# Optimization experiments

Hardware: AMD Instinct MI355X
Metric: run time of the kernel (lower is better)

Reference implementation:

```python
import jax, jax.numpy as jnp
import numpy as np

SPATIAL = (14, 14)
FEATURE_DIM = 768
N, T, H, D = 16, 8, 12, 64
L = SPATIAL[0] * SPATIAL[1] + 1  # 197 (cls token + 196 patches)
W_SIZE = (2 * SPATIAL[0] - 1) * (2 * SPATIAL[1] - 1)  # 729


def _build_idx():
    # relative-position index map [196, 196], matches the torch double loop
    hs, ws = SPATIAL
    pos = np.arange(hs * ws)
    pi, pj = pos // ws, pos % ws
    i_offs = pi[:, None] - pi[None, :] + hs - 1
    j_offs = pj[:, None] - pj[None, :] + ws - 1
    return jnp.asarray(i_offs * (2 * ws - 1) + j_offs, dtype=jnp.int32)


def setup_inputs() -> dict:
    key = jax.random.key(0)
    kq, kk, kw1, kw2 = jax.random.split(key, 4)
    q = jax.random.normal(kq, (N, T, L, H, D), dtype=jnp.float32)
    k = jax.random.normal(kk, (N, T, L, H, D), dtype=jnp.float32)
    # learned relative-position bias tables (zeros in torch init; use small random for a meaningful baseline)
    w1 = jax.random.normal(kw1, (W_SIZE, FEATURE_DIM), dtype=jnp.float32) * 0.02
    w2 = jax.random.normal(kw2, (W_SIZE, FEATURE_DIM), dtype=jnp.float32) * 0.02
    idx = _build_idx()
    return {"q": q, "k": k, "w1": w1, "w2": w2, "idx": idx}


def _forward_half(q, k, w, idx):
    # q, k: [N, T', L, H, D]; strip cls token -> [N, T', 196, H, D]
    q = q[:, :, 1:]
    k = k[:, :, 1:]
    scale = 1.0 / jnp.sqrt(jnp.asarray(q.shape[-1], q.dtype))
    attn = jnp.einsum('ntqhd,ntkhd->ntqkh', q * scale, k)
    attn = jax.nn.softmax(attn, axis=-2).mean(axis=-1)  # [N, T', 196, 196]
    w_unroll = w[idx]  # gather: [196, 196, C]
    return jnp.einsum('ntqk,qkc->ntqc', attn, w_unroll)


def reference(q, k, w1, w2, idx):
    n, t, l, _, _ = q.shape
    c = w1.shape[-1]
    ret = jnp.zeros((n, t, l, c), dtype=q.dtype)
    ret = ret.at[:, 1:, 1:, :].add(_forward_half(q[:, 1:], k[:, :-1], w1, idx))
    ret = ret.at[:, :-1, 1:, :].add(_forward_half(q[:, :-1], k[:, 1:], w2, idx))
    return ret
```

## Files before the change

### kernel.cpp

```cpp
#include <hip/hip_runtime.h>

#define N_ 16
#define T_ 8
#define L_ 197
#define H_ 12
#define D_ 64
#define Q_ 196
#define C_ 768
#define KP 224
#define ENT 1792
#define ATS 216
#define APLANE 2112

typedef unsigned short ushort_t;
typedef __bf16 bf16x8 __attribute__((ext_vector_type(8)));
typedef float floatx4 __attribute__((ext_vector_type(4)));

#define GLD_LDS16(g, l)                                                    \
  __builtin_amdgcn_global_load_lds(                                        \
      (const __attribute__((address_space(1))) void*)(g),                  \
      (__attribute__((address_space(3))) void*)(l), 16, 0, 0)

static __device__ inline ushort_t f2bf(float x) {
  unsigned int u = __float_as_uint(x);
  u += 0x7fffu + ((u >> 16) & 1u);
  return (ushort_t)(u >> 16);
}
static __device__ inline unsigned int pack2(float a, float b) {
  return (unsigned int)f2bf(a) | ((unsigned int)f2bf(b) << 16);
}

__global__ __launch_bounds__(256, 4) void convert_kernel(
    const float* __restrict__ q, const float* __restrict__ k,
    uint4* __restrict__ qb, uint4* __restrict__ kb) {
  const int nt  = blockIdx.x;
  const int h   = blockIdx.y;
  const int inp = blockIdx.z;
  const int tid = threadIdx.x;

  const float* src = inp ? k : q;
  const float sc = inp ? 1.f : 0.125f;
  uint4* dst = (inp ? kb : qb) + ((size_t)nt * H_ + h) * ENT;

  __shared__ __align__(16) uint4 lds[8 * KP];

  const float* base = src + ((size_t)nt * L_ + 1) * (H_ * D_) + h * D_;

  float4 va[7], vb[7];
  #pragma unroll
  for (int r = 0; r < 7; r++) {
    int e = tid + 256 * r;
    int pos = e >> 3, dc = e & 7;
    if (r < 6 || tid < 32) {
      const float* p = base + (size_t)pos * (H_ * D_) + dc * 8;
      va[r] = *(const float4*)p;
      vb[r] = *(const float4*)(p + 4);
    }
  }
  __builtin_amdgcn_sched_barrier(0);

  #pragma unroll
  for (int r = 0; r < 7; r++) {
    int e = tid + 256 * r;
    int pos = e >> 3, dc = e & 7;
    if (r < 6 || tid < 32) {
      uint4 o;
      o.x = pack2(va[r].x * sc, va[r].y * sc);
      o.y = pack2(va[r].z * sc, va[r].w * sc);
      o.z = pack2(vb[r].x * sc, vb[r].y * sc);
      o.w = pack2(vb[r].z * sc, vb[r].w * sc);
      lds[dc * KP + ((pos & ~7) | ((pos ^ dc) & 7))] = o;
    }
  }
  __syncthreads();

  #pragma unroll
  for (int r = 0; r < 7; r++) {
    int e = tid + 256 * r;
    int dc = e / KP, pos = e - dc * KP;
    uint4 v;
    if (pos < 196) v = lds[dc * KP + ((pos & ~7) | ((pos ^ dc) & 7))];
    else           v = (uint4){0u, 0u, 0u, 0u};
    dst[e] = v;
  }
}

__global__ __launch_bounds__(256, 2) void attn_kernel(
    const uint4* __restrict__ qb, const uint4* __restrict__ kb,
    ushort_t* __restrict__ A1, ushort_t* __restrict__ A2) {
  const int lin  = blockIdx.x;
  const int xcd  = lin & 7;
  const int slot = lin >> 3;
  const int g    = (slot >> 2) * 8 + xcd;
  const int b    = slot & 3;
  const int half = g / 112;
  const int nt   = g - half * 112;
  const int n  = nt / 7, tp = nt % 7;
  const int tq = (half == 0) ? tp + 1 : tp;
  const int tk = (half == 0) ? tp     : tp + 1;
  const int ntq = n * T_ + tq;
  const int ntk = n * T_ + tk;

  const uint4* qpl = qb + (size_t)ntq * H_ * ENT;
  const uint4* kpl = kb + (size_t)ntk * H_ * ENT;
  ushort_t* Ah = (half == 0) ? A1 : A2;

  __shared__ __align__(16) uint4 ks[2][ENT];
  ushort_t* at = (ushort_t*)ks;

  const int tid  = threadIdx.x;
  const int lane = tid & 63;
  const int wv   = tid >> 6;
  const int quad = lane >> 4;
  const int l15  = lane & 15;
  const int qi_b = 64 * b + 16 * wv;

  float accA[13][4];
  #pragma unroll
  for (int t = 0; t < 13; t++)
    #pragma unroll
    for (int r = 0; r < 4; r++) accA[t][r] = 0.f;

  auto stage = [&](int h, uint4* bufp) {
    #pragma unroll
    for (int r = 0; r < 7; r++)
      GLD_LDS16(kpl + (size_t)h * ENT + 256 * r + 64 * wv + lane,
                (char*)bufp + (256 * r + 64 * wv) * 16);
  };
  auto loadq = [&](int h, bf16x8* qf) {
    #pragma unroll
    for (int kk = 0; kk < 2; kk++)
      qf[kk] = *(const bf16x8*)&qpl[(size_t)h * ENT + (quad + 4 * kk) * KP + qi_b + l15];
  };

  auto headbody = [&](int h, uint4* bufp, bf16x8* qf, bool lastwait) {
    if (lastwait) asm volatile("s_waitcnt vmcnt(0)" ::: "memory");
    else          asm volatile("s_waitcnt vmcnt(9)" ::: "memory");
    __builtin_amdgcn_s_barrier();
    asm volatile("" ::: "memory");

    const ushort_t* bu = (const ushort_t*)bufp;
    floatx4 S[13];
    #pragma unroll
    for (int t = 0; t < 13; t++) S[t] = (floatx4){0.f, 0.f, 0.f, 0.f};
    #pragma unroll
    for (int kk = 0; kk < 2; kk++)
      #pragma unroll
      for (int t = 0; t < 13; t++) {
        bf16x8 bbv = *(const bf16x8*)&bu[((quad + 4 * kk) * KP + 16 * t + l15) * 8];
        S[t] = __builtin_amdgcn_mfma_f32_16x16x32_bf16(qf[kk], bbv, S[t], 0, 0, 0);
      }

    asm volatile("" ::: "memory");
    __builtin_amdgcn_s_barrier();
    if (h + 2 < H_) {
      loadq(h + 2, qf);
      stage(h + 2, bufp);
      __builtin_amdgcn_sched_barrier(0);
    }

    #pragma unroll
    for (int r = 0; r < 4; r++) {
      float s = 0.f;
      #pragma unroll
      for (int t = 0; t < 13; t++) {
        float e_ = (t == 12 && l15 >= 4) ? 0.f : __expf(S[t][r]);
        S[t][r] = e_;
        s += e_;
      }
      #pragma unroll
      for (int off = 1; off < 16; off <<= 1) s += __shfl_xor(s, off);
      float inv = 1.f / s;
      #pragma unroll
      for (int t = 0; t < 13; t++) accA[t][r] += S[t][r] * inv;
    }
  };

  bf16x8 qfA[2], qfB[2];
  loadq(0, qfA); stage(0, ks[0]);
  __builtin_amdgcn_sched_barrier(0);
  loadq(1, qfB); stage(1, ks[1]);
  __builtin_amdgcn_sched_barrier(0);

  #pragma unroll 1
  for (int hh = 0; hh < 6; hh++) {
    headbody(2 * hh,     ks[0], qfA, false);
    headbody(2 * hh + 1, ks[1], qfB, hh == 5);
  }

  const float s12 = 1.f / 12.f;
  #pragma unroll
  for (int t = 0; t < 13; t++)
    #pragma unroll
    for (int r = 0; r < 4; r++)
      at[(16 * wv + 4 * quad + r) * ATS + 16 * t + l15] = f2bf(accA[t][r] * s12);
  #pragma unroll
  for (int i = 0; i < 7; i++) {
    int e = lane + 64 * i;
    if (e < 416) {
      int row = e / 26, col = e - row * 26;
      uint4 v = *(const uint4*)&at[(16 * wv + row) * ATS + col * 8];
      int qi = qi_b + row;
      if (qi < Q_)
        *(uint4*)(Ah + ((size_t)qi * (N_ * T_) + ntq) * KP + col * 8) = v;
    }
  }
}

__global__ __launch_bounds__(256, 4) void mix_kernel(
    const ushort_t* __restrict__ A1, const ushort_t* __restrict__ A2,
    const float* __restrict__ w1, const float* __restrict__ w2,
    const int* __restrict__ idx, float* __restrict__ out) {
  const int ct = blockIdx.x;
  const int qi = blockIdx.y;
  const int tid  = threadIdx.x;
  const int lane = tid & 63;
  const int wv   = tid >> 6;
  const int quad = lane >> 4;
  const int l15  = lane & 15;
  const int p    = lane >> 2;
  const int cq   = lane & 3;

  __shared__ __align__(16) char As[2][4 * APLANE];
  __shared__ ushort_t Ws[128][40];

  int idxr0[7], idxr1[7];
  #pragma unroll
  for (int kc = 0; kc < 7; kc++) {
    int off = 32 * kc + 2 * p;
    if (off > 194) off = 194;
    int2 pr = *(const int2*)(idx + (size_t)qi * Q_ + off);
    idxr0[kc] = pr.x; idxr1[kc] = pr.y;
  }

  floatx4 acc[8][2];
  #pragma unroll
  for (int mt = 0; mt < 8; mt++)
    #pragma unroll
    for (int u = 0; u < 2; u++) acc[mt][u] = (floatx4){0.f, 0.f, 0.f, 0.f};

  float4 pw[2][2];
  const int cbase = ct * 128 + wv * 32;

  {
    const ushort_t* Ah_ = A1;
    #pragma unroll
    for (int r = 0; r < 2; r++)
      GLD_LDS16(Ah_ + ((size_t)qi * 128 + r * 64 + lane) * KP + wv * 8,
                As[0] + wv * APLANE + r * 1024);
    #pragma unroll
    for (int j = 0; j < 2; j++)
      #pragma unroll
      for (int u = 0; u < 2; u++)
        pw[j][u] = *(const float4*)(w1 + (size_t)(j ? idxr1[0] : idxr0[0]) * C_ +
                                    cbase + (cq + 4 * u) * 4);
  }

  #pragma unroll
  for (int ht = 0; ht < 14; ht++) {
    const int half = ht / 7, kc = ht % 7;
    __syncthreads();

    #pragma unroll
    for (int u = 0; u < 2; u++) {
      const float* f0 = (const float*)&pw[0][u];
      const float* f1 = (const float*)&pw[1][u];
      #pragma unroll
      for (int e = 0; e < 4; e++)
        *(unsigned int*)&Ws[wv * 32 + (cq + 4 * u) * 4 + e][2 * p] = pack2(f0[e], f1[e]);
    }

    if (ht + 1 < 14) {
      const int nh = (ht + 1) / 7, nk = (ht + 1) % 7;
      const ushort_t* Ah_ = nh ? A2 : A1;
      const float* w_ = nh ? w2 : w1;
      #pragma unroll
      for (int r = 0; r < 2; r++)
        GLD_LDS16(Ah_ + ((size_t)qi * 128 + r * 64 + lane) * KP + 32 * nk + wv * 8,
                  As[(ht + 1) & 1] + wv * APLANE + r * 1024);
      int r0 = idxr0[nk], r1 = idxr1[nk];
      #pragma unroll
      for (int u = 0; u < 2; u++) {
        pw[0][u] = *(const float4*)(w_ + (size_t)r0 * C_ + cbase + (cq + 4 * u) * 4);
        pw[1][u] = *(const float4*)(w_ + (size_t)r1 * C_ + cbase + (cq + 4 * u) * 4);
      }
    }

    const char* ab = As[ht & 1];
    bf16x8 bfv[2];
    #pragma unroll
    for (int u = 0; u < 2; u++)
      bfv[u] = *(const bf16x8*)&Ws[wv * 32 + 16 * u + l15][8 * quad];
    #pragma unroll
    for (int mt = 0; mt < 8; mt++) {
      bf16x8 a = *(const bf16x8*)(ab + quad * APLANE + (16 * mt + l15) * 16);
      acc[mt][0] = __builtin_amdgcn_mfma_f32_16x16x32_bf16(a, bfv[0], acc[mt][0], 0, 0, 0);
      acc[mt][1] = __builtin_amdgcn_mfma_f32_16x16x32_bf16(a, bfv[1], acc[mt][1], 0, 0, 0);
    }
  }

  #pragma unroll
  for (int u = 0; u < 2; u++) {
    const int c = ct * 128 + 32 * wv + 16 * u + l15;
    #pragma unroll
    for (int mt = 0; mt < 8; mt++)
      #pragma unroll
      for (int r = 0; r < 4; r++) {
        int m = 16 * mt + 4 * quad + r;
        out[((size_t)m * L_ + 1 + qi) * C_ + c] = acc[mt][u][r];
      }
  }
  if (qi == 0) {
    #pragma unroll
    for (int u = 0; u < 2; u++) {
      const int c = ct * 128 + 32 * wv + 16 * u + l15;
      #pragma unroll
      for (int mt = 0; mt < 8; mt++)
        #pragma unroll
        for (int r = 0; r < 4; r++) {
          int m = 16 * mt + 4 * quad + r;
          out[(size_t)m * L_ * C_ + c] = 0.f;
        }
    }
  }
}

extern "C" void kernel_launch(void* const* d_in, const int* in_sizes, int n_in,
                              void* d_out, int out_size, void* d_ws, size_t ws_size,
                              hipStream_t stream) {
  const float* q  = (const float*)d_in[0];
  const float* k  = (const float*)d_in[1];
  const float* w1 = (const float*)d_in[2];
  const float* w2 = (const float*)d_in[3];
  const int* idx  = (const int*)d_in[4];
  float* out = (float*)d_out;

  const size_t plane_tot = (size_t)(N_ * T_) * H_ * ENT;
  uint4* qb = (uint4*)d_ws;
  uint4* kb = qb + plane_tot;
  ushort_t* A1 = (ushort_t*)(kb + plane_tot);
  size_t Aelems = (size_t)Q_ * (N_ * T_) * KP;
  ushort_t* A2 = A1 + Aelems;

  hipMemsetAsync(A1, 0, Aelems * 2 * sizeof(ushort_t), stream);

  convert_kernel<<<dim3(N_ * T_, H_, 2), 256, 0, stream>>>(q, k, qb, kb);
  attn_kernel<<<dim3(896), 256, 0, stream>>>(qb, kb, A1, A2);
  mix_kernel<<<dim3(6, Q_), 256, 0, stream>>>(A1, A2, w1, w2, idx, out);
}
```

Before: 336.5 us.

## Deepen K-loop prefetch to two stages with manual vmcnt waits and barriers

Restructures the main loop so the W-table gather and the A-tile global-to-LDS DMA are issued two iterations ahead, using two register buffers and both LDS buffers in rotation. The implicit full __syncthreads is replaced by explicit s_waitcnt vmcnt(6) plus raw s_barrier pairs around the LDS reads, which lets one chunk's loads stay in flight during compute. This aims to hide global-load latency behind the MFMAs, at the cost of more registers for the second prefetch buffer. The hand-set vmcnt counts have to match the exact number of outstanding loads the compiler emits.

```diff
diff --git a/kernel.cpp b/kernel.cpp
--- a/kernel.cpp
+++ b/kernel.cpp
@@ -239,64 +239,73 @@
     #pragma unroll
     for (int u = 0; u < 2; u++) acc[mt][u] = (floatx4){0.f, 0.f, 0.f, 0.f};
 
-  float4 pw[2][2];
   const int cbase = ct * 128 + wv * 32;
 
-  {
-    const ushort_t* Ah_ = A1;
+  auto gather = [&](int ch, float4 (&pw)[2][2]) {
+    const float* w_ = (ch >= 7) ? w2 : w1;
+    const int nk = ch % 7;
+    const int r0 = idxr0[nk], r1 = idxr1[nk];
+    #pragma unroll
+    for (int u = 0; u < 2; u++) {
+      pw[0][u] = *(const float4*)(w_ + (size_t)r0 * C_ + cbase + (cq + 4 * u) * 4);
+      pw[1][u] = *(const float4*)(w_ + (size_t)r1 * C_ + cbase + (cq + 4 * u) * 4);
+    }
+  };
+  auto dma = [&](int ch, char* buf) {
+    const ushort_t* Ah_ = (ch >= 7) ? A2 : A1;
+    const int nk = ch % 7;
     #pragma unroll
     for (int r = 0; r < 2; r++)
-      GLD_LDS16(Ah_ + ((size_t)qi * 128 + r * 64 + lane) * KP + wv * 8,
-                As[0] + wv * APLANE + r * 1024);
-    #pragma unroll
-    for (int j = 0; j < 2; j++)
-      #pragma unroll
-      for (int u = 0; u < 2; u++)
-        pw[j][u] = *(const float4*)(w1 + (size_t)(j ? idxr1[0] : idxr0[0]) * C_ +
-                                    cbase + (cq + 4 * u) * 4);
-  }
-
-  #pragma unroll
-  for (int ht = 0; ht < 14; ht++) {
-    const int half = ht / 7, kc = ht % 7;
-    __syncthreads();
+      GLD_LDS16(Ah_ + ((size_t)qi * 128 + r * 64 + lane) * KP + 32 * nk + wv * 8,
+                buf + wv * APLANE + r * 1024);
+  };
+
+  float4 pwA[2][2], pwB[2][2];
+  gather(0, pwA); dma(0, As[0]);
+  __builtin_amdgcn_sched_barrier(0);
+  gather(1, pwB); dma(1, As[1]);
+  __builtin_amdgcn_sched_barrier(0);
+
+  auto body = [&](int ht, char* bufp, float4 (&pwX)[2][2], bool lastwait) {
+    if (lastwait) asm volatile("s_waitcnt vmcnt(0)" ::: "memory");
+    else          asm volatile("s_waitcnt vmcnt(6)" ::: "memory");
 
     #pragma unroll
     for (int u = 0; u < 2; u++) {
-      const float* f0 = (const float*)&pw[0][u];
-      const float* f1 = (const float*)&pw[1][u];
+      const float* f0 = (const float*)&pwX[0][u];
+      const float* f1 = (const float*)&pwX[1][u];
       #pragma unroll
       for (int e = 0; e < 4; e++)
         *(unsigned int*)&Ws[wv * 32 + (cq + 4 * u) * 4 + e][2 * p] = pack2(f0[e], f1[e]);
     }
 
-    if (ht + 1 < 14) {
-      const int nh = (ht + 1) / 7, nk = (ht + 1) % 7;
-      const ushort_t* Ah_ = nh ? A2 : A1;
-      const float* w_ = nh ? w2 : w1;
-      #pragma unroll
-      for (int r = 0; r < 2; r++)
-        GLD_LDS16(Ah_ + ((size_t)qi * 128 + r * 64 + lane) * KP + 32 * nk + wv * 8,
-                  As[(ht + 1) & 1] + wv * APLANE + r * 1024);
-      int r0 = idxr0[nk], r1 = idxr1[nk];
-      #pragma unroll
-      for (int u = 0; u < 2; u++) {
-        pw[0][u] = *(const float4*)(w_ + (size_t)r0 * C_ + cbase + (cq + 4 * u) * 4);
-        pw[1][u] = *(const float4*)(w_ + (size_t)r1 * C_ + cbase + (cq + 4 * u) * 4);
-      }
-    }
-
-    const char* ab = As[ht & 1];
+    __builtin_amdgcn_s_barrier();
+    asm volatile("" ::: "memory");
+
     bf16x8 bfv[2];
     #pragma unroll
     for (int u = 0; u < 2; u++)
       bfv[u] = *(const bf16x8*)&Ws[wv * 32 + 16 * u + l15][8 * quad];
     #pragma unroll
     for (int mt = 0; mt < 8; mt++) {
-      bf16x8 a = *(const bf16x8*)(ab + quad * APLANE + (16 * mt + l15) * 16);
+      bf16x8 a = *(const bf16x8*)(bufp + quad * APLANE + (16 * mt + l15) * 16);
       acc[mt][0] = __builtin_amdgcn_mfma_f32_16x16x32_bf16(a, bfv[0], acc[mt][0], 0, 0, 0);
       acc[mt][1] = __builtin_amdgcn_mfma_f32_16x16x32_bf16(a, bfv[1], acc[mt][1], 0, 0, 0);
     }
+
+    asm volatile("" ::: "memory");
+    __builtin_amdgcn_s_barrier();
+    if (ht + 2 < 14) {
+      gather(ht + 2, pwX);
+      dma(ht + 2, bufp);
+      __builtin_amdgcn_sched_barrier(0);
+    }
+  };
+
+  #pragma unroll
+  for (int ht = 0; ht < 14; ht++) {
+    if (ht & 1) body(ht, As[1], pwB, ht == 13);
+    else        body(ht, As[0], pwA, false);
   }
 
   #pragma unroll
```

New measurement: 360.8 us. 7.2% more time.
